# Kernel optimization log

Measured on AMD Instinct MI355X. Metric: run time of the kernel, lower is better.

The kernel has to match this reference:

```python
import jax, jax.numpy as jnp
import numpy as np

DIM = 1024
HEADS = 16
HEAD_DIM = DIM // HEADS
SCALE = DIM ** -0.5  # note: original uses full dim, not head_dim


def setup_inputs() -> dict:
    key = jax.random.key(0)
    k1, k2, k3, k4 = jax.random.split(key, 4)
    x = jax.random.normal(k1, (4, 2048, DIM), dtype=jnp.float32)
    # nn.Linear(dim, 3*dim, bias=False): weight [3*dim, dim]; y = x @ W.T
    w_qkv = jax.random.normal(k2, (3 * DIM, DIM), dtype=jnp.float32) * (DIM ** -0.5)
    w_out = jax.random.normal(k3, (DIM, DIM), dtype=jnp.float32) * (DIM ** -0.5)
    b_out = jax.random.normal(k4, (DIM,), dtype=jnp.float32) * 0.01
    return {"x": x, "w_qkv": w_qkv, "w_out": w_out, "b_out": b_out}


def reference(x, w_qkv, w_out, b_out):
    b, n, d = x.shape
    qkv = jnp.einsum('bnd,ed->bne', x, w_qkv)  # [b, n, 3*dim]
    # rearrange 'b n (qkv h d) -> qkv b h n d'
    qkv = qkv.reshape(b, n, 3, HEADS, HEAD_DIM).transpose(2, 0, 3, 1, 4)
    q, k, v = qkv[0], qkv[1], qkv[2]
    dots = jnp.einsum('bhid,bhjd->bhij', q, k) * SCALE
    attn = jax.nn.softmax(dots, axis=-1)
    out = jnp.einsum('bhij,bhjd->bhid', attn, v)
    out = out.transpose(0, 2, 1, 3).reshape(b, n, d)  # b h n d -> b n (h d)
    return jnp.einsum('bnd,ed->bne', out, w_out) + b_out
```

## Files before the change

### kernel.cpp

```cpp
#include <hip/hip_runtime.h>
#include <stdint.h>
#include <stddef.h>

typedef _Float16 f16;
typedef __attribute__((ext_vector_type(8))) _Float16 f16x8;
typedef __attribute__((ext_vector_type(4))) _Float16 f16x4;
typedef __attribute__((ext_vector_type(4))) float f32x4;

#define DINL __device__ __forceinline__

DINL void async_cp16(void* lds, const void* gmem) {
    __builtin_amdgcn_global_load_lds(
        (const __attribute__((address_space(1))) void*)(uintptr_t)gmem,
        (__attribute__((address_space(3))) void*)(uint32_t)(uintptr_t)lds,
        16, 0, 0);
}

__global__ void cast_fused(const float* __restrict__ x, f16* __restrict__ xh,
                           const float* __restrict__ wq, f16* __restrict__ wqh,
                           const float* __restrict__ wo, f16* __restrict__ woh,
                           float qs) {
    int stride = gridDim.x * blockDim.x;
    for (int i = blockIdx.x * blockDim.x + threadIdx.x; i < 3145728; i += stride) {
        const float4* src; f16x4* dst; float s = 1.f;
        if (i < 2097152)      { src = (const float4*)x  + i;            dst = (f16x4*)xh  + i; }
        else if (i < 2883584) { int j = i - 2097152; src = (const float4*)wq + j; dst = (f16x4*)wqh + j;
                                if (j < 262144) s = qs; }
        else                  { int j = i - 2883584; src = (const float4*)wo + j; dst = (f16x4*)woh + j; }
        float4 v = *src;
        f16x4 h = { (f16)(v.x * s), (f16)(v.y * s), (f16)(v.z * s), (f16)(v.w * s) };
        *dst = h;
    }
}

template <typename TC, bool HAS_BIAS>
__global__ __launch_bounds__(256) void gemm_bt(
    const f16* __restrict__ A, const f16* __restrict__ B,
    TC* __restrict__ C, const float* __restrict__ bias,
    int M, int N, int K)
{
    constexpr int BK = 64;
    __shared__ __align__(16) f16 As[128 * BK];
    __shared__ __align__(16) f16 Bs[128 * BK];

    const int tid  = threadIdx.x;
    const int lane = tid & 63;
    const int wave = tid >> 6;
    const int bm = blockIdx.y * 128;
    const int bn = blockIdx.x * 128;
    const int wr = (wave >> 1) * 64;
    const int wc = (wave & 1) * 64;

    f32x4 acc[4][4] = {};

    for (int k0 = 0; k0 < K; k0 += BK) {
#pragma unroll
        for (int it = 0; it < 4; ++it) {
            int s = tid + it * 256, row = s >> 3, cc = (s & 7) ^ (row & 7);
            async_cp16(&As[(size_t)s * 8], &A[(size_t)(bm + row) * K + k0 + cc * 8]);
        }
#pragma unroll
        for (int it = 0; it < 4; ++it) {
            int s = tid + it * 256, row = s >> 3, cc = (s & 7) ^ (row & 7);
            async_cp16(&Bs[(size_t)s * 8], &B[(size_t)(bn + row) * K + k0 + cc * 8]);
        }
        __syncthreads();

#pragma unroll
        for (int ks = 0; ks < BK; ks += 32) {
            const int rlo = lane & 15;
            const int c = (ks >> 3) + (lane >> 4);
            f16x8 af[4], bf[4];
#pragma unroll
            for (int m = 0; m < 4; ++m) {
                int r = wr + m * 16 + rlo;
                af[m] = *(const f16x8*)&As[(r * 8 + (c ^ (r & 7))) * 8];
            }
#pragma unroll
            for (int n = 0; n < 4; ++n) {
                int r = wc + n * 16 + rlo;
                bf[n] = *(const f16x8*)&Bs[(r * 8 + (c ^ (r & 7))) * 8];
            }
#pragma unroll
            for (int m = 0; m < 4; ++m)
#pragma unroll
                for (int n = 0; n < 4; ++n)
                    acc[m][n] = __builtin_amdgcn_mfma_f32_16x16x32_f16(af[m], bf[n], acc[m][n], 0, 0, 0);
        }
        __syncthreads();
    }

#pragma unroll
    for (int n = 0; n < 4; ++n) {
        const int gc = bn + wc + n * 16 + (lane & 15);
        float bv = 0.f;
        if constexpr (HAS_BIAS) bv = bias[gc];
#pragma unroll
        for (int m = 0; m < 4; ++m) {
            const int gr0 = bm + wr + m * 16 + ((lane >> 4) << 2);
#pragma unroll
            for (int r = 0; r < 4; ++r) {
                float v = acc[m][n][r] + bv;
                if constexpr (sizeof(TC) == 4) C[(size_t)(gr0 + r) * N + gc] = v;
                else                           C[(size_t)(gr0 + r) * N + gc] = (f16)v;
            }
        }
    }
}

__global__ __launch_bounds__(256) void transpose_v(const f16* __restrict__ qkv, f16* __restrict__ vt) {
    __shared__ float T[64][65];
    const int bid = blockIdx.x, bh = bid >> 5, st = bid & 31;
    const int b = bh >> 4, h = bh & 15, s0 = st * 64;
    const int tid = threadIdx.x;
    const int rs = tid >> 2, c0 = (tid & 3) * 16;
    const f16* src = &qkv[(size_t)(b * 2048 + s0 + rs) * 3072 + 2048 + h * 64 + c0];
    f16x8 v0 = ((const f16x8*)src)[0], v1 = ((const f16x8*)src)[1];
#pragma unroll
    for (int e = 0; e < 8; ++e) { T[rs][c0 + e] = (float)v0[e]; T[rs][c0 + 8 + e] = (float)v1[e]; }
    __syncthreads();
    const int rd = tid >> 2, k0 = (tid & 3) * 16;
    f16x8 w0, w1;
#pragma unroll
    for (int e = 0; e < 8; ++e) { w0[e] = (f16)T[k0 + e][rd]; w1[e] = (f16)T[k0 + 8 + e][rd]; }
    f16* dst = &vt[(size_t)(bh * 64 + rd) * 2048 + s0 + k0];
    ((f16x8*)dst)[0] = w0; ((f16x8*)dst)[1] = w1;
}

DINL void stage_kv(f16* Kd, f16* Vd, const f16* qkv, const f16* vt,
                   size_t base, int bh, int jt, int tid) {
    int s = tid, row = s >> 3, cc = (s & 7) ^ (row & 7);
    int s2 = tid + 256, row2 = s2 >> 3, cc2 = (s2 & 7) ^ (row2 & 7);
    async_cp16(&Kd[s * 8],  &qkv[base + 1024 + (size_t)(jt * 64 + row)  * 3072 + cc * 8]);
    async_cp16(&Kd[s2 * 8], &qkv[base + 1024 + (size_t)(jt * 64 + row2) * 3072 + cc2 * 8]);
    async_cp16(&Vd[s * 8],  &vt[(size_t)(bh * 64 + row)  * 2048 + jt * 64 + cc * 8]);
    async_cp16(&Vd[s2 * 8], &vt[(size_t)(bh * 64 + row2) * 2048 + jt * 64 + cc2 * 8]);
}

__global__ __launch_bounds__(256, 4) void attn_mfma(
    const f16* __restrict__ qkv, const f16* __restrict__ vt, f16* __restrict__ out)
{
    constexpr int TD = 3072;
    __shared__ __align__(16) f16 Ks[2][64 * 64];
    __shared__ __align__(16) f16 Vs[2][64 * 64];
    __shared__ __align__(16) f16 Ps[4][16 * 64];

    const int tid = threadIdx.x, lane = tid & 63, wave = tid >> 6;
    const int bh = blockIdx.x, b = bh >> 4, h = bh & 15;
    const int q0 = blockIdx.y * 64;
    const size_t base = (size_t)b * 2048 * TD + h * 64;
    const int lo = lane & 15, hi = lane >> 4, ml = lo & 7;

    const f16* qp = &qkv[base + (size_t)(q0 + wave * 16 + lo) * TD + hi * 8];
    f16x8 qf0 = *(const f16x8*)qp;
    f16x8 qf1 = *(const f16x8*)(qp + 32);

    stage_kv(Ks[0], Vs[0], qkv, vt, base, bh, 0, tid);

    float lsum = 0.f;
    f32x4 o_[4] = {};
    char* Pb = (char*)&Ps[wave][0];

    for (int jt = 0; jt < 32; ++jt) {
        const int cur = jt & 1;
        __syncthreads();
        if (jt + 1 < 32)
            stage_kv(Ks[cur ^ 1], Vs[cur ^ 1], qkv, vt, base, bh, jt + 1, tid);

        f32x4 sc[4] = {};
#pragma unroll
        for (int ks = 0; ks < 2; ++ks) {
            const int c = ks * 4 + hi;
            const f16x8 qf = ks ? qf1 : qf0;
#pragma unroll
            for (int n = 0; n < 4; ++n) {
                int key = n * 16 + lo;
                f16x8 kf = *(const f16x8*)&Ks[cur][(key * 8 + (c ^ (key & 7))) * 8];
                sc[n] = __builtin_amdgcn_mfma_f32_16x16x32_f16(kf, qf, sc[n], 0, 0, 0);
            }
        }

#pragma unroll
        for (int n = 0; n < 4; ++n) {
            float p0 = exp2f(sc[n][0]), p1 = exp2f(sc[n][1]);
            float p2 = exp2f(sc[n][2]), p3 = exp2f(sc[n][3]);
            lsum += (p0 + p1) + (p2 + p3);
            f16x4 h4 = { (f16)p0, (f16)p1, (f16)p2, (f16)p3 };
            *(f16x4*)(Pb + ((lo * 128 + hi * 8 + n * 32) ^ (ml << 4))) = h4;
        }
        asm volatile("s_waitcnt lgkmcnt(0)" ::: "memory");

#pragma unroll
        for (int ks = 0; ks < 2; ++ks) {
            const int c = ks * 4 + hi;
            f16x8 pa = *(const f16x8*)(Pb + ((lo * 128 + c * 16) ^ (ml << 4)));
#pragma unroll
            for (int n = 0; n < 4; ++n) {
                int dd = n * 16 + lo;
                f16x8 vb = *(const f16x8*)&Vs[cur][(dd * 8 + (c ^ (dd & 7))) * 8];
                o_[n] = __builtin_amdgcn_mfma_f32_16x16x32_f16(pa, vb, o_[n], 0, 0, 0);
            }
        }
    }

    lsum += __shfl_xor(lsum, 16);
    lsum += __shfl_xor(lsum, 32);
#pragma unroll
    for (int r = 0; r < 4; ++r) {
        float inv = 1.f / __shfl(lsum, hi * 4 + r);
        int row = q0 + wave * 16 + hi * 4 + r;
#pragma unroll
        for (int n = 0; n < 4; ++n) {
            int dim = h * 64 + n * 16 + lo;
            out[(size_t)(b * 2048 + row) * 1024 + dim] = (f16)(o_[n][r] * inv);
        }
    }
}

extern "C" void kernel_launch(void* const* d_in, const int* in_sizes, int n_in,
                              void* d_out, int out_size, void* d_ws, size_t ws_size,
                              hipStream_t stream)
{
    int ix = 0, iq = 1, iw = 2, ib = 3;
    for (int i = 0; i < n_in; ++i) {
        if      (in_sizes[i] == 8388608) ix = i;
        else if (in_sizes[i] == 3145728) iq = i;
        else if (in_sizes[i] == 1048576) iw = i;
        else if (in_sizes[i] == 1024)    ib = i;
    }
    const float* x     = (const float*)d_in[ix];
    const float* w_qkv = (const float*)d_in[iq];
    const float* w_out = (const float*)d_in[iw];
    const float* b_out = (const float*)d_in[ib];

    char* ws = (char*)d_ws;
    f16* Xh    = (f16*)(ws + 0);
    f16* AOh   = Xh;
    f16* Wqkvh = (f16*)(ws + 16777216);
    f16* QKVh  = (f16*)(ws + 23068672);
    f16* Vth   = (f16*)(ws + 73400320);
    f16* Wouth = (f16*)(ws + 90177536);

    const float QSCALE = 0.03125f * 1.4426950408889634f;

    cast_fused<<<3072, 256, 0, stream>>>(x, Xh, w_qkv, Wqkvh, w_out, Wouth, QSCALE);

    gemm_bt<f16, false><<<dim3(24, 64), 256, 0, stream>>>(
        Xh, Wqkvh, QKVh, nullptr, 8192, 3072, 1024);

    transpose_v<<<2048, 256, 0, stream>>>(QKVh, Vth);

    attn_mfma<<<dim3(64, 32), 256, 0, stream>>>(QKVh, Vth, AOh);

    gemm_bt<float, true><<<dim3(8, 64), 256, 0, stream>>>(
        AOh, Wouth, (float*)d_out, b_out, 8192, 1024, 1024);
}
```

Before: 322.2 us.

## Keep softmax probabilities in registers by permuting key rows on load

```diff
diff --git a/kernel.cpp b/kernel.cpp
--- a/kernel.cpp
+++ b/kernel.cpp
@@ -127,45 +127,53 @@
     ((f16x8*)dst)[0] = w0; ((f16x8*)dst)[1] = w1;
 }
 
-DINL void stage_kv(f16* Kd, f16* Vd, const f16* qkv, const f16* vt,
-                   size_t base, int bh, int jt, int tid) {
-    int s = tid, row = s >> 3, cc = (s & 7) ^ (row & 7);
-    int s2 = tid + 256, row2 = s2 >> 3, cc2 = (s2 & 7) ^ (row2 & 7);
-    async_cp16(&Kd[s * 8],  &qkv[base + 1024 + (size_t)(jt * 64 + row)  * 3072 + cc * 8]);
-    async_cp16(&Kd[s2 * 8], &qkv[base + 1024 + (size_t)(jt * 64 + row2) * 3072 + cc2 * 8]);
-    async_cp16(&Vd[s * 8],  &vt[(size_t)(bh * 64 + row)  * 2048 + jt * 64 + cc * 8]);
-    async_cp16(&Vd[s2 * 8], &vt[(size_t)(bh * 64 + row2) * 2048 + jt * 64 + cc2 * 8]);
-}
-
-__global__ __launch_bounds__(256, 4) void attn_mfma(
+DINL int phi_row(int r) {
+    return (r & 32) | ((r & 12) << 1) | ((r & 16) >> 2) | (r & 3);
+}
+
+__global__ __launch_bounds__(256, 5) void attn_mfma(
     const f16* __restrict__ qkv, const f16* __restrict__ vt, f16* __restrict__ out)
 {
     constexpr int TD = 3072;
+    constexpr int KSTR = 64 * TD;
     __shared__ __align__(16) f16 Ks[2][64 * 64];
     __shared__ __align__(16) f16 Vs[2][64 * 64];
-    __shared__ __align__(16) f16 Ps[4][16 * 64];
 
     const int tid = threadIdx.x, lane = tid & 63, wave = tid >> 6;
     const int bh = blockIdx.x, b = bh >> 4, h = bh & 15;
     const int q0 = blockIdx.y * 64;
     const size_t base = (size_t)b * 2048 * TD + h * 64;
-    const int lo = lane & 15, hi = lane >> 4, ml = lo & 7;
+    const int lo = lane & 15, hi = lane >> 4;
 
     const f16* qp = &qkv[base + (size_t)(q0 + wave * 16 + lo) * TD + hi * 8];
     f16x8 qf0 = *(const f16x8*)qp;
     f16x8 qf1 = *(const f16x8*)(qp + 32);
 
-    stage_kv(Ks[0], Vs[0], qkv, vt, base, bh, 0, tid);
+    const int s1 = tid,        r1 = s1 >> 3, c1 = (s1 & 7) ^ (r1 & 7);
+    const int s2 = tid + 256,  r2 = s2 >> 3, c2 = (s2 & 7) ^ (r2 & 7);
+    const f16* kg1 = &qkv[base + 1024 + (size_t)phi_row(r1) * TD + c1 * 8];
+    const f16* kg2 = &qkv[base + 1024 + (size_t)phi_row(r2) * TD + c2 * 8];
+    const f16* vg1 = &vt[(size_t)(bh * 64 + r1) * 2048 + c1 * 8];
+    const f16* vg2 = &vt[(size_t)(bh * 64 + r2) * 2048 + c2 * 8];
+    f16* kd1 = &Ks[0][s1 * 8]; f16* kd2 = &Ks[0][s2 * 8];
+    f16* vd1 = &Vs[0][s1 * 8]; f16* vd2 = &Vs[0][s2 * 8];
+
+    async_cp16(kd1, kg1); async_cp16(kd2, kg2);
+    async_cp16(vd1, vg1); async_cp16(vd2, vg2);
+    kg1 += KSTR; kg2 += KSTR; vg1 += 64; vg2 += 64;
 
     float lsum = 0.f;
     f32x4 o_[4] = {};
-    char* Pb = (char*)&Ps[wave][0];
 
     for (int jt = 0; jt < 32; ++jt) {
         const int cur = jt & 1;
         __syncthreads();
-        if (jt + 1 < 32)
-            stage_kv(Ks[cur ^ 1], Vs[cur ^ 1], qkv, vt, base, bh, jt + 1, tid);
+        if (jt + 1 < 32) {
+            const int nb = (cur ^ 1) * 4096;
+            async_cp16(kd1 + nb, kg1); async_cp16(kd2 + nb, kg2);
+            async_cp16(vd1 + nb, vg1); async_cp16(vd2 + nb, vg2);
+            kg1 += KSTR; kg2 += KSTR; vg1 += 64; vg2 += 64;
+        }
 
         f32x4 sc[4] = {};
 #pragma unroll
@@ -174,26 +182,27 @@
             const f16x8 qf = ks ? qf1 : qf0;
 #pragma unroll
             for (int n = 0; n < 4; ++n) {
-                int key = n * 16 + lo;
-                f16x8 kf = *(const f16x8*)&Ks[cur][(key * 8 + (c ^ (key & 7))) * 8];
+                int kr = n * 16 + lo;
+                f16x8 kf = *(const f16x8*)&Ks[cur][(kr * 8 + (c ^ (kr & 7))) * 8];
                 sc[n] = __builtin_amdgcn_mfma_f32_16x16x32_f16(kf, qf, sc[n], 0, 0, 0);
             }
         }
 
+        f16x8 pa0, pa1;
 #pragma unroll
         for (int n = 0; n < 4; ++n) {
             float p0 = exp2f(sc[n][0]), p1 = exp2f(sc[n][1]);
             float p2 = exp2f(sc[n][2]), p3 = exp2f(sc[n][3]);
             lsum += (p0 + p1) + (p2 + p3);
-            f16x4 h4 = { (f16)p0, (f16)p1, (f16)p2, (f16)p3 };
-            *(f16x4*)(Pb + ((lo * 128 + hi * 8 + n * 32) ^ (ml << 4))) = h4;
-        }
-        asm volatile("s_waitcnt lgkmcnt(0)" ::: "memory");
+            const int off = (n & 1) * 4;
+            if (n < 2) { pa0[off] = (f16)p0; pa0[off+1] = (f16)p1; pa0[off+2] = (f16)p2; pa0[off+3] = (f16)p3; }
+            else       { pa1[off] = (f16)p0; pa1[off+1] = (f16)p1; pa1[off+2] = (f16)p2; pa1[off+3] = (f16)p3; }
+        }
 
 #pragma unroll
         for (int ks = 0; ks < 2; ++ks) {
             const int c = ks * 4 + hi;
-            f16x8 pa = *(const f16x8*)(Pb + ((lo * 128 + c * 16) ^ (ml << 4)));
+            const f16x8 pa = ks ? pa1 : pa0;
 #pragma unroll
             for (int n = 0; n < 4; ++n) {
                 int dd = n * 16 + lo;
```

Result: faster. 290.3 us (-9.9%).
